# Kernel optimization log

Hardware: AMD Instinct MI355X
Metric: run time of the kernel (lower is better)

Reference implementation:

```python
import math
import jax, jax.numpy as jnp
import numpy as np

B, S, H, I, E = 4, 2048, 1024, 4096, 8
CAPACITY_FACTOR = 1.0


def setup_inputs() -> dict:
    key = jax.random.key(0)
    k1, k2, k3, k4, k5 = jax.random.split(key, 5)
    x = jax.random.normal(k1, (B, S, H), dtype=jnp.float32)
    # Router: nn.Linear(H, E) with xavier_uniform weight, zero-ish bias
    limit = math.sqrt(6.0 / (H + E))
    router_w = jax.random.uniform(k2, (E, H), dtype=jnp.float32, minval=-limit, maxval=limit)
    router_b = jnp.zeros((E,), dtype=jnp.float32)
    # Expert weights (torch.randn init; scaled for numeric sanity)
    experts_inter = jax.random.normal(k3, (E, H, I), dtype=jnp.float32) * 0.02
    experts_out = jax.random.normal(k4, (E, I, H), dtype=jnp.float32) * 0.02
    return {"x": x, "router_w": router_w, "router_b": router_b,
            "experts_inter": experts_inter, "experts_out": experts_out}


def reference(x, router_w, router_b, experts_inter, experts_out):
    b, s, h = x.shape
    e = experts_inter.shape[0]
    capacity = math.ceil(b * s / e * CAPACITY_FACTOR)  # static

    # Router: linear + softmax over experts
    routing_weights = jax.nn.softmax(x @ router_w.T + router_b, axis=-1)  # [b,s,e]

    x_flat = x.reshape(-1, h)                       # [N, h]
    w_flat = routing_weights.reshape(-1, e)         # [N, e]

    # softmax > 0 everywhere, but keep faithful mask-based routing
    routing_mask = (w_flat > 0).astype(jnp.int32)   # [N, e]
    # stable descending sort per expert column (matches stable torch.sort)
    sorted_indices = jnp.argsort(-routing_mask, axis=0, stable=True)  # [N, e]
    sorted_mask = jnp.take_along_axis(routing_mask, sorted_indices, axis=0)[:capacity]  # [c, e]
    sorted_indices = sorted_indices[:capacity]      # [c, e]

    used_tokens_indices = (sorted_indices * sorted_mask).reshape(-1)  # [c*e]
    mask_f = sorted_mask.reshape(-1).astype(x.dtype)[:, None]
    inputs_tokens = x_flat[used_tokens_indices] * mask_f              # [c*e, h]
    inputs_tokens = inputs_tokens.reshape(capacity, e, h)             # [c, e, h]
    inputs_weights = jnp.take_along_axis(w_flat, sorted_indices, axis=0)  # [c, e]

    # grouped expert FFN
    inter = jnp.einsum('ceh,ehi->cei', inputs_tokens, experts_inter)  # [c, e, I]
    inter = jax.nn.relu(inter)
    out = jnp.einsum('cei,eih->ceh', inter, experts_out)              # [c, e, h]
    out = out * inputs_weights[..., None]
    out = out.reshape(-1, h)                                          # [c*e, h]

    # scatter-add combine
    combined = jnp.zeros_like(x_flat).at[used_tokens_indices].add(out)
    return combined.reshape(b, s, h)
```

## Files before the change

### kernel.cpp

```cpp
#include <hip/hip_runtime.h>
#include <stdint.h>

#define H_DIM 1024
#define I_DIM 4096
#define E_NUM 8
#define CAP   1024

typedef __attribute__((ext_vector_type(8))) short bf16x8;
typedef __attribute__((ext_vector_type(4))) float f32x4;

#define AS1 __attribute__((address_space(1)))
#define AS3 __attribute__((address_space(3)))

__device__ __forceinline__ unsigned short f2bf(float f){
  union { float f; uint32_t u; } v; v.f = f;
  uint32_t u = v.u;
  uint32_t r = (u + 0x7FFFu + ((u >> 16) & 1u)) >> 16;
  return (unsigned short)r;
}

__global__ __launch_bounds__(256) void prep_kernel(
    const float* __restrict__ x, const float* __restrict__ rw_w,
    const float* __restrict__ rb, const float* __restrict__ w1,
    float* __restrict__ out, int n4,
    unsigned short* __restrict__ xb, float* __restrict__ rwout,
    unsigned short* __restrict__ wt)
{
  __shared__ float smem[64][65];
  int bid = blockIdx.x;
  int t   = threadIdx.x;

  if (bid < 1024){
    float4 z; z.x=0.f; z.y=0.f; z.z=0.f; z.w=0.f;
    float4* p = (float4*)out;
    for (int i = bid*256 + t; i < n4; i += 1024*256) p[i] = z;
    return;
  }
  if (bid < 2048){
    int c = bid - 1024;
    const float* xr = x + (size_t)c*H_DIM;
    float4 xv = *(const float4*)(xr + t*4);
    ushort4 xo;
    xo.x = f2bf(xv.x); xo.y = f2bf(xv.y); xo.z = f2bf(xv.z); xo.w = f2bf(xv.w);
    *(ushort4*)(xb + (size_t)c*H_DIM + t*4) = xo;
    float acc[E_NUM];
    #pragma unroll
    for (int e=0;e<E_NUM;e++){
      float4 wv = *(const float4*)(rw_w + e*H_DIM + t*4);
      acc[e] = xv.x*wv.x + xv.y*wv.y + xv.z*wv.z + xv.w*wv.w;
    }
    float (*part)[E_NUM] = (float (*)[E_NUM])smem;
    #pragma unroll
    for (int e=0;e<E_NUM;e++) part[t][e]=acc[e];
    __syncthreads();
    for (int s=128; s>0; s>>=1){
      if (t<s){
        #pragma unroll
        for (int e=0;e<E_NUM;e++) part[t][e]+=part[t+s][e];
      }
      __syncthreads();
    }
    if (t==0){
      float l[E_NUM], mx=-1e30f;
      #pragma unroll
      for (int e=0;e<E_NUM;e++){ l[e]=part[0][e]+rb[e]; mx=fmaxf(mx,l[e]); }
      float s=0.f;
      #pragma unroll
      for (int e=0;e<E_NUM;e++){ l[e]=expf(l[e]-mx); s+=l[e]; }
      float inv = 1.f/s;
      #pragma unroll
      for (int e=0;e<E_NUM;e++) rwout[c*E_NUM+e] = l[e]*inv;
    }
    return;
  }
  int idx = bid - 2048;
  int e   = idx >> 10;
  int rem = idx & 1023;
  int by  = rem >> 6, bx = rem & 63;
  const float* src = w1 + (size_t)e*H_DIM*I_DIM;
  unsigned short* dst = wt + (size_t)e*I_DIM*H_DIM;
  int c0 = bx*64, r0 = by*64;
  int tx = t & 15, ty = t >> 4;
  #pragma unroll
  for (int p=0;p<4;p++){
    int r = ty + p*16;
    float4 v = *(const float4*)(src + (size_t)(r0+r)*I_DIM + c0 + tx*4);
    smem[r][tx*4+0]=v.x; smem[r][tx*4+1]=v.y; smem[r][tx*4+2]=v.z; smem[r][tx*4+3]=v.w;
  }
  __syncthreads();
  #pragma unroll
  for (int p=0;p<4;p++){
    int c = ty + p*16;
    ushort4 o;
    o.x = f2bf(smem[tx*4+0][c]);
    o.y = f2bf(smem[tx*4+1][c]);
    o.z = f2bf(smem[tx*4+2][c]);
    o.w = f2bf(smem[tx*4+3][c]);
    *(ushort4*)(dst + (size_t)(c0+c)*H_DIM + r0 + tx*4) = o;
  }
}

__global__ __launch_bounds__(256) void transpose_cvt64(
    const float* __restrict__ src, unsigned short* __restrict__ dst,
    int R, int C, long srcZ, long dstZ)
{
  src += (size_t)blockIdx.z * srcZ;
  dst += (size_t)blockIdx.z * dstZ;
  __shared__ float tile[64][65];
  int c0 = blockIdx.x*64, r0 = blockIdx.y*64;
  int t  = threadIdx.x;
  int tx = t & 15, ty = t >> 4;
  #pragma unroll
  for (int p=0;p<4;p++){
    int r = ty + p*16;
    float4 v = *(const float4*)(src + (size_t)(r0+r)*C + c0 + tx*4);
    tile[r][tx*4+0]=v.x; tile[r][tx*4+1]=v.y; tile[r][tx*4+2]=v.z; tile[r][tx*4+3]=v.w;
  }
  __syncthreads();
  #pragma unroll
  for (int p=0;p<4;p++){
    int c = ty + p*16;
    ushort4 o;
    o.x = f2bf(tile[tx*4+0][c]);
    o.y = f2bf(tile[tx*4+1][c]);
    o.z = f2bf(tile[tx*4+2][c]);
    o.w = f2bf(tile[tx*4+3][c]);
    *(ushort4*)(dst + (size_t)(c0+c)*R + r0 + tx*4) = o;
  }
}

template<int MODE>
__global__ __launch_bounds__(512, 4) void gemm_s(
    const unsigned short* __restrict__ A, int lda, long aZ,
    const unsigned short* __restrict__ B, int ldb, long bZ,
    int NS, int tilesPerZ,
    const float* __restrict__ rw,
    unsigned short* __restrict__ outInter,
    float* __restrict__ outAdd)
{
  __shared__ unsigned short As[128*64];
  __shared__ unsigned short Bs[256*64];

  int nwg = gridDim.x;
  int id  = blockIdx.x;
  int swz = (id & 7)*(nwg >> 3) + (id >> 3);
  int z   = swz / tilesPerZ;
  int rr_ = swz - z*tilesPerZ;
  int mt  = rr_ & 7, nt = rr_ >> 3;
  int m0  = mt*128, n0 = nt*256;

  const unsigned short* Ab = A + (size_t)z*aZ + (size_t)m0*lda;
  const unsigned short* Bb = B + (size_t)z*bZ + (size_t)n0*ldb;

  int tid  = threadIdx.x;
  int w    = tid >> 6, l = tid & 63;
  int wr   = w >> 2,  wc = w & 3;
  int lrow = l & 15,  lq = l >> 4;
  int r7   = lrow & 7;

  int srow = l >> 3;
  int sg   = ((l & 7) ^ ((l >> 3) & 7)) * 8;

  f32x4 acc[4][4];
  #pragma unroll
  for (int i=0;i<4;i++)
    #pragma unroll
    for (int j=0;j<4;j++)
      acc[i][j] = (f32x4){0.f,0.f,0.f,0.f};

  for (int s=0; s<NS; ++s){
    int kt = s*64;
    #pragma unroll
    for (int i=0;i<2;i++){
      int rbase = w*16 + i*8;
      __builtin_amdgcn_global_load_lds(
        (const AS1 void*)(Ab + (size_t)(rbase + srow)*lda + kt + sg),
        (AS3 void*)((char*)As + rbase*128), 16, 0, 0);
    }
    #pragma unroll
    for (int i=0;i<4;i++){
      int rbase = w*32 + i*8;
      __builtin_amdgcn_global_load_lds(
        (const AS1 void*)(Bb + (size_t)(rbase + srow)*ldb + kt + sg),
        (AS3 void*)((char*)Bs + rbase*128), 16, 0, 0);
    }
    __syncthreads();

    #pragma unroll
    for (int kk=0;kk<2;kk++){
      bf16x8 af[4], bfr[4];
      int slot = ((kk*4 + lq) ^ r7) << 4;
      #pragma unroll
      for (int f=0;f<4;f++)
        af[f]  = *(const bf16x8*)((const char*)As + (wr*64 + f*16 + lrow)*128 + slot);
      #pragma unroll
      for (int f=0;f<4;f++)
        bfr[f] = *(const bf16x8*)((const char*)Bs + (wc*64 + f*16 + lrow)*128 + slot);
      __builtin_amdgcn_s_setprio(1);
      #pragma unroll
      for (int fm=0;fm<4;fm++)
        #pragma unroll
        for (int fn=0;fn<4;fn++)
          acc[fm][fn] = __builtin_amdgcn_mfma_f32_16x16x32_bf16(af[fm], bfr[fn], acc[fm][fn], 0, 0, 0);
      __builtin_amdgcn_s_setprio(0);
    }

    __syncthreads();
  }

  #pragma unroll
  for (int fm=0;fm<4;fm++){
    #pragma unroll
    for (int fn=0;fn<4;fn++){
      #pragma unroll
      for (int rg=0;rg<4;rg++){
        int gm = m0 + wr*64 + fm*16 + lq*4 + rg;
        int gn = n0 + wc*64 + fn*16 + lrow;
        float v = acc[fm][fn][rg];
        if (MODE==0){
          v = fmaxf(v, 0.f) * rw[gm*E_NUM + z];
          outInter[(size_t)gm*(E_NUM*I_DIM) + (size_t)z*I_DIM + gn] = f2bf(v);
        } else {
          atomicAdd(&outAdd[(size_t)gm*H_DIM + gn], v);
        }
      }
    }
  }
}

extern "C" void kernel_launch(void* const* d_in, const int* in_sizes, int n_in,
                              void* d_out, int out_size, void* d_ws, size_t ws_size,
                              hipStream_t stream)
{
  const float* x   = (const float*)d_in[0];
  const float* rww = (const float*)d_in[1];
  const float* rwb = (const float*)d_in[2];
  const float* w1  = (const float*)d_in[3];
  const float* w2  = (const float*)d_in[4];
  float* out = (float*)d_out;

  char* ws = (char*)d_ws;
  float*          rwout = (float*)(ws);
  unsigned short* xb    = (unsigned short*)(ws + (1u<<16));
  unsigned short* inter = (unsigned short*)(ws + (4ull<<20));
  unsigned short* wt    = (unsigned short*)(ws + (68ull<<20));
  const size_t needed = 132ull<<20;

  if (ws_size < needed){
    prep_kernel<<<1024, 256, 0, stream>>>(x, rww, rwb, w1, out, out_size/4,
                                          xb, rwout, wt);
    return;
  }

  prep_kernel<<<10240, 256, 0, stream>>>(x, rww, rwb, w1, out, out_size/4,
                                         xb, rwout, wt);

  gemm_s<0><<<1024, 512, 0, stream>>>(
      xb, H_DIM, 0L,
      wt, H_DIM, (long)I_DIM*H_DIM,
      16, 128, rwout, inter, nullptr);

  transpose_cvt64<<<dim3(H_DIM/64, (E_NUM*I_DIM)/64, 1), 256, 0, stream>>>(
      w2, wt, E_NUM*I_DIM, H_DIM, 0L, 0L);

  gemm_s<1><<<512, 512, 0, stream>>>(
      inter, E_NUM*I_DIM, 2048L,
      wt,    E_NUM*I_DIM, 2048L,
      32, 32, nullptr, nullptr, out);
}
```

Before: 247.8 us.

## Overlap W2 transpose-convert with first expert GEMM in one launch

Interleaves transpose-and-convert workgroups for the second expert weight matrix into the first GEMM's grid, one in every three blocks, writing into a separate workspace buffer. The memory-bound conversion then runs alongside the compute-bound GEMM instead of as a separate launch in between. It also removes the s_setprio hints around the MFMA loops and specialises the GEMM kernels with constant strides. It needs 64 MB more workspace and falls back to the old sequence when that is unavailable.

```diff
diff --git a/kernel.cpp b/kernel.cpp
--- a/kernel.cpp
+++ b/kernel.cpp
@@ -100,12 +100,134 @@
   }
 }
 
+__global__ __launch_bounds__(512, 4) void gemm1_fused(
+    const unsigned short* __restrict__ A,
+    const unsigned short* __restrict__ B,
+    const float* __restrict__ rw,
+    unsigned short* __restrict__ outInter,
+    const float* __restrict__ w2,
+    unsigned short* __restrict__ w2t,
+    int fused)
+{
+  __shared__ char ldsbuf[49152];
+  int id  = blockIdx.x;
+  int tid = threadIdx.x;
+  int gid = id;
+
+  if (fused){
+    if ((id % 3) == 2){
+      int tb = id / 3;
+      float (*tile)[65] = (float (*)[65])ldsbuf;
+      int r0 = tb*64;
+      int tx = tid & 15, ty = tid >> 4;
+      for (int j=0; j<16; ++j){
+        int c0 = j*64;
+        #pragma unroll
+        for (int p=0;p<2;p++){
+          int r = ty + p*32;
+          float4 v = *(const float4*)(w2 + (size_t)(r0+r)*H_DIM + c0 + tx*4);
+          tile[r][tx*4+0]=v.x; tile[r][tx*4+1]=v.y; tile[r][tx*4+2]=v.z; tile[r][tx*4+3]=v.w;
+        }
+        __syncthreads();
+        #pragma unroll
+        for (int p=0;p<2;p++){
+          int c = ty + p*32;
+          ushort4 o;
+          o.x = f2bf(tile[tx*4+0][c]);
+          o.y = f2bf(tile[tx*4+1][c]);
+          o.z = f2bf(tile[tx*4+2][c]);
+          o.w = f2bf(tile[tx*4+3][c]);
+          *(ushort4*)(w2t + (size_t)(c0+c)*(E_NUM*I_DIM) + r0 + tx*4) = o;
+        }
+        __syncthreads();
+      }
+      return;
+    }
+    gid = (id/3)*2 + (id%3);
+  }
+
+  unsigned short* As = (unsigned short*)ldsbuf;
+  unsigned short* Bs = (unsigned short*)(ldsbuf + 16384);
+  int swz = (gid & 7)*128 + (gid >> 3);
+  int z   = swz >> 7;
+  int rr_ = swz & 127;
+  int mt  = rr_ & 7, nt = rr_ >> 3;
+  int m0  = mt*128, n0 = nt*256;
+
+  const unsigned short* Ab = A + (size_t)m0*H_DIM;
+  const unsigned short* Bb = B + (size_t)z*I_DIM*H_DIM + (size_t)n0*H_DIM;
+
+  int w    = tid >> 6, l = tid & 63;
+  int wr   = w >> 2,  wc = w & 3;
+  int lrow = l & 15,  lq = l >> 4;
+  int r7   = lrow & 7;
+  int srow = l >> 3;
+  int sg   = ((l & 7) ^ ((l >> 3) & 7)) * 8;
+
+  f32x4 acc[4][4];
+  #pragma unroll
+  for (int i=0;i<4;i++)
+    #pragma unroll
+    for (int j=0;j<4;j++)
+      acc[i][j] = (f32x4){0.f,0.f,0.f,0.f};
+
+  for (int s=0; s<16; ++s){
+    int kt = s*64;
+    #pragma unroll
+    for (int i=0;i<2;i++){
+      int rbase = w*16 + i*8;
+      __builtin_amdgcn_global_load_lds(
+        (const AS1 void*)(Ab + (size_t)(rbase + srow)*H_DIM + kt + sg),
+        (AS3 void*)((char*)As + rbase*128), 16, 0, 0);
+    }
+    #pragma unroll
+    for (int i=0;i<4;i++){
+      int rbase = w*32 + i*8;
+      __builtin_amdgcn_global_load_lds(
+        (const AS1 void*)(Bb + (size_t)(rbase + srow)*H_DIM + kt + sg),
+        (AS3 void*)((char*)Bs + rbase*128), 16, 0, 0);
+    }
+    __syncthreads();
+
+    #pragma unroll
+    for (int kk=0;kk<2;kk++){
+      bf16x8 af[4], bfr[4];
+      int slot = ((kk*4 + lq) ^ r7) << 4;
+      #pragma unroll
+      for (int f=0;f<4;f++)
+        af[f]  = *(const bf16x8*)((const char*)As + (wr*64 + f*16 + lrow)*128 + slot);
+      #pragma unroll
+      for (int f=0;f<4;f++)
+        bfr[f] = *(const bf16x8*)((const char*)Bs + (wc*64 + f*16 + lrow)*128 + slot);
+      #pragma unroll
+      for (int fm=0;fm<4;fm++)
+        #pragma unroll
+        for (int fn=0;fn<4;fn++)
+          acc[fm][fn] = __builtin_amdgcn_mfma_f32_16x16x32_bf16(af[fm], bfr[fn], acc[fm][fn], 0, 0, 0);
+    }
+
+    __syncthreads();
+  }
+
+  #pragma unroll
+  for (int fm=0;fm<4;fm++){
+    #pragma unroll
+    for (int fn=0;fn<4;fn++){
+      #pragma unroll
+      for (int rg=0;rg<4;rg++){
+        int gm = m0 + wr*64 + fm*16 + lq*4 + rg;
+        int gn = n0 + wc*64 + fn*16 + lrow;
+        float v = fmaxf(acc[fm][fn][rg], 0.f) * rw[gm*E_NUM + z];
+        outInter[(size_t)gm*(E_NUM*I_DIM) + (size_t)z*I_DIM + gn] = f2bf(v);
+      }
+    }
+  }
+}
+
 __global__ __launch_bounds__(256) void transpose_cvt64(
     const float* __restrict__ src, unsigned short* __restrict__ dst,
-    int R, int C, long srcZ, long dstZ)
-{
-  src += (size_t)blockIdx.z * srcZ;
-  dst += (size_t)blockIdx.z * dstZ;
+    int R, int C)
+{
   __shared__ float tile[64][65];
   int c0 = blockIdx.x*64, r0 = blockIdx.y*64;
   int t  = threadIdx.x;
@@ -129,13 +251,9 @@
   }
 }
 
-template<int MODE>
-__global__ __launch_bounds__(512, 4) void gemm_s(
-    const unsigned short* __restrict__ A, int lda, long aZ,
-    const unsigned short* __restrict__ B, int ldb, long bZ,
-    int NS, int tilesPerZ,
-    const float* __restrict__ rw,
-    unsigned short* __restrict__ outInter,
+__global__ __launch_bounds__(512, 4) void gemm2_k(
+    const unsigned short* __restrict__ A,
+    const unsigned short* __restrict__ B,
     float* __restrict__ outAdd)
 {
   __shared__ unsigned short As[128*64];
@@ -144,20 +262,20 @@
   int nwg = gridDim.x;
   int id  = blockIdx.x;
   int swz = (id & 7)*(nwg >> 3) + (id >> 3);
-  int z   = swz / tilesPerZ;
-  int rr_ = swz - z*tilesPerZ;
+  int z   = swz >> 5;
+  int rr_ = swz & 31;
   int mt  = rr_ & 7, nt = rr_ >> 3;
   int m0  = mt*128, n0 = nt*256;
-
-  const unsigned short* Ab = A + (size_t)z*aZ + (size_t)m0*lda;
-  const unsigned short* Bb = B + (size_t)z*bZ + (size_t)n0*ldb;
+  const int ld = E_NUM*I_DIM;
+
+  const unsigned short* Ab = A + (size_t)z*2048 + (size_t)m0*ld;
+  const unsigned short* Bb = B + (size_t)z*2048 + (size_t)n0*ld;
 
   int tid  = threadIdx.x;
   int w    = tid >> 6, l = tid & 63;
   int wr   = w >> 2,  wc = w & 3;
   int lrow = l & 15,  lq = l >> 4;
   int r7   = lrow & 7;
-
   int srow = l >> 3;
   int sg   = ((l & 7) ^ ((l >> 3) & 7)) * 8;
 
@@ -168,20 +286,20 @@
     for (int j=0;j<4;j++)
       acc[i][j] = (f32x4){0.f,0.f,0.f,0.f};
 
-  for (int s=0; s<NS; ++s){
+  for (int s=0; s<32; ++s){
     int kt = s*64;
     #pragma unroll
     for (int i=0;i<2;i++){
       int rbase = w*16 + i*8;
       __builtin_amdgcn_global_load_lds(
-        (const AS1 void*)(Ab + (size_t)(rbase + srow)*lda + kt + sg),
+        (const AS1 void*)(Ab + (size_t)(rbase + srow)*ld + kt + sg),
         (AS3 void*)((char*)As + rbase*128), 16, 0, 0);
     }
     #pragma unroll
     for (int i=0;i<4;i++){
       int rbase = w*32 + i*8;
       __builtin_amdgcn_global_load_lds(
-        (const AS1 void*)(Bb + (size_t)(rbase + srow)*ldb + kt + sg),
+        (const AS1 void*)(Bb + (size_t)(rbase + srow)*ld + kt + sg),
         (AS3 void*)((char*)Bs + rbase*128), 16, 0, 0);
     }
     __syncthreads();
@@ -196,13 +314,11 @@
       #pragma unroll
       for (int f=0;f<4;f++)
         bfr[f] = *(const bf16x8*)((const char*)Bs + (wc*64 + f*16 + lrow)*128 + slot);
-      __builtin_amdgcn_s_setprio(1);
       #pragma unroll
       for (int fm=0;fm<4;fm++)
         #pragma unroll
         for (int fn=0;fn<4;fn++)
           acc[fm][fn] = __builtin_amdgcn_mfma_f32_16x16x32_bf16(af[fm], bfr[fn], acc[fm][fn], 0, 0, 0);
-      __builtin_amdgcn_s_setprio(0);
     }
 
     __syncthreads();
@@ -216,13 +332,7 @@
       for (int rg=0;rg<4;rg++){
         int gm = m0 + wr*64 + fm*16 + lq*4 + rg;
         int gn = n0 + wc*64 + fn*16 + lrow;
-        float v = acc[fm][fn][rg];
-        if (MODE==0){
-          v = fmaxf(v, 0.f) * rw[gm*E_NUM + z];
-          outInter[(size_t)gm*(E_NUM*I_DIM) + (size_t)z*I_DIM + gn] = f2bf(v);
-        } else {
-          atomicAdd(&outAdd[(size_t)gm*H_DIM + gn], v);
-        }
+        atomicAdd(&outAdd[(size_t)gm*H_DIM + gn], acc[fm][fn][rg]);
       }
     }
   }
@@ -244,7 +354,9 @@
   unsigned short* xb    = (unsigned short*)(ws + (1u<<16));
   unsigned short* inter = (unsigned short*)(ws + (4ull<<20));
   unsigned short* wt    = (unsigned short*)(ws + (68ull<<20));
-  const size_t needed = 132ull<<20;
+  unsigned short* w2t   = (unsigned short*)(ws + (132ull<<20));
+  const size_t needed      = 132ull<<20;
+  const size_t needed_big  = 196ull<<20;
 
   if (ws_size < needed){
     prep_kernel<<<1024, 256, 0, stream>>>(x, rww, rwb, w1, out, out_size/4,
@@ -255,16 +367,13 @@
   prep_kernel<<<10240, 256, 0, stream>>>(x, rww, rwb, w1, out, out_size/4,
                                          xb, rwout, wt);
 
-  gemm_s<0><<<1024, 512, 0, stream>>>(
-      xb, H_DIM, 0L,
-      wt, H_DIM, (long)I_DIM*H_DIM,
-      16, 128, rwout, inter, nullptr);
-
-  transpose_cvt64<<<dim3(H_DIM/64, (E_NUM*I_DIM)/64, 1), 256, 0, stream>>>(
-      w2, wt, E_NUM*I_DIM, H_DIM, 0L, 0L);
-
-  gemm_s<1><<<512, 512, 0, stream>>>(
-      inter, E_NUM*I_DIM, 2048L,
-      wt,    E_NUM*I_DIM, 2048L,
-      32, 32, nullptr, nullptr, out);
-}
+  if (ws_size >= needed_big){
+    gemm1_fused<<<1536, 512, 0, stream>>>(xb, wt, rwout, inter, w2, w2t, 1);
+    gemm2_k<<<512, 512, 0, stream>>>(inter, w2t, out);
+  } else {
+    gemm1_fused<<<1024, 512, 0, stream>>>(xb, wt, rwout, inter, w2, wt, 0);
+    transpose_cvt64<<<dim3(H_DIM/64, (E_NUM*I_DIM)/64), 256, 0, stream>>>(
+        w2, wt, E_NUM*I_DIM, H_DIM);
+    gemm2_k<<<512, 512, 0, stream>>>(inter, wt, out);
+  }
+}
```

Measured after the change: 263.0 us. 1.06x slower.
